# Optimization experiments

Hardware: AMD Instinct MI355X
Metric: run time of the kernel (lower is better)

## Reference

```python
import jax, jax.numpy as jnp
import numpy as np

B, IN, H = 4096, 1024, 1024


def setup_inputs() -> dict:
    key = jax.random.key(0)
    ks = jax.random.split(key, 12)
    s = float(np.sqrt(6.0 / (IN + H)))  # xavier-uniform-like scale
    u = lambda k, shp: jax.random.uniform(k, shp, jnp.float32, -s, s)
    return {
        "x": jax.random.normal(ks[0], (B, IN), jnp.float32),
        "h_prev": jax.random.normal(ks[1], (B, H), jnp.float32),
        "c_prev": jax.random.normal(ks[2], (B, H), jnp.float32),
        "n_prev": jnp.ones((B, H), jnp.float32),
        "m_prev": jnp.zeros((B, H), jnp.float32),
        "Wi_x": u(ks[3], (H, IN)), "bi": jnp.zeros((H,), jnp.float32), "Wi_h": u(ks[4], (H, H)),
        "Wf_x": u(ks[5], (H, IN)), "bf": jnp.full((H,), 2.0, jnp.float32), "Wf_h": u(ks[6], (H, H)),
        "Wz_x": u(ks[7], (H, IN)), "bz": jnp.zeros((H,), jnp.float32), "Wz_h": u(ks[8], (H, H)),
        "Wo_x": u(ks[9], (H, IN)), "bo": jnp.zeros((H,), jnp.float32), "Wo_h": u(ks[10], (H, H)),
    }


def reference(x, h_prev, c_prev, n_prev, m_prev,
              Wi_x, bi, Wi_h, Wf_x, bf, Wf_h,
              Wz_x, bz, Wz_h, Wo_x, bo, Wo_h):
    # 8 projections (x-side with bias, h-side without), torch Linear: y = x @ W.T + b
    i_tilde = x @ Wi_x.T + bi + h_prev @ Wi_h.T
    f_aff   = x @ Wf_x.T + bf + h_prev @ Wf_h.T
    z_aff   = x @ Wz_x.T + bz + h_prev @ Wz_h.T
    o_aff   = x @ Wo_x.T + bo + h_prev @ Wo_h.T

    # forget_as_exp=False path: sigmoid forget gate, log-domain stabilizer
    log_f = jnp.log(jnp.clip(jax.nn.sigmoid(f_aff), 1e-8, None))
    m_t = jnp.maximum(log_f + m_prev, i_tilde)
    i_prime = jnp.exp(i_tilde - m_t)
    f_prime = jnp.exp(log_f + m_prev - m_t)

    z = jnp.tanh(z_aff)
    c_t = f_prime * c_prev + i_prime * z
    n_t = f_prime * n_prev + i_prime
    h_t = jax.nn.sigmoid(o_aff) * (c_t / jnp.clip(n_t, 1e-6, None))
    return h_t, c_t, n_t, m_t
```

## Files before the change

### kernel.cpp

```cpp
#include <hip/hip_runtime.h>
#include <stdint.h>


#define B_DIM 4096
#define K_DIM 2048

typedef __bf16 bf16x8 __attribute__((ext_vector_type(8)));
typedef float f32x4 __attribute__((ext_vector_type(4)));
typedef unsigned short ushort8 __attribute__((ext_vector_type(8)));

__device__ __forceinline__ unsigned short f2bf(float f) {
  unsigned u = __float_as_uint(f);
  u += 0x7fffu + ((u >> 16) & 1u);
  return (unsigned short)(u >> 16);
}
__device__ __forceinline__ float bf2f(unsigned short u) {
  return __uint_as_float(((unsigned)u) << 16);
}

__device__ __forceinline__ ushort8 load8_as_bf16(const void* base, size_t off, bool isbf) {
  if (isbf) return *(const ushort8*)((const unsigned short*)base + off);
  const float* f = (const float*)base + off;
  float4 v0 = ((const float4*)f)[0];
  float4 v1 = ((const float4*)f)[1];
  ushort8 o;
  o[0] = f2bf(v0.x); o[1] = f2bf(v0.y); o[2] = f2bf(v0.z); o[3] = f2bf(v0.w);
  o[4] = f2bf(v1.x); o[5] = f2bf(v1.y); o[6] = f2bf(v1.z); o[7] = f2bf(v1.w);
  return o;
}

__global__ void pack_all(const void* __restrict__ xv, const void* __restrict__ hv,
                         const void* __restrict__ Wix, const void* __restrict__ Wih,
                         const void* __restrict__ Wfx, const void* __restrict__ Wfh,
                         const void* __restrict__ Wzx, const void* __restrict__ Wzh,
                         const void* __restrict__ Wox, const void* __restrict__ Woh,
                         unsigned short* __restrict__ Apk, unsigned short* __restrict__ Bpk) {
  const int blk = blockIdx.x;
  const int lane = threadIdx.x & 63;
  const bool isA = blk < 4096;
  const unsigned* disc = (const unsigned*)(isA ? xv : Wix);
  int v = 0;
  if (lane < 32) {
    unsigned e = (disc[lane] >> 7) & 0xFFu;
    v = (e > (isA ? 129u : 122u)) ? 1 : 0;
  }
  const bool isbf = (__ballot(v) == 0ull);

  const int k = threadIdx.x * 8;
  if (isA) {
    const int m = blk;
    const void* src = (k < 1024) ? xv : hv;
    size_t off = (size_t)m * 1024 + (k & 1023);
    *(ushort8*)(Apk + (size_t)m * 2048 + k) = load8_as_bf16(src, off, isbf);
  } else {
    const int br = blk - 4096;
    const int g = (br >> 4) & 3;
    const int wrow = ((br >> 6) << 4) | (br & 15);
    const void* W;
    if (k < 1024) W = (g == 0) ? Wix : (g == 1) ? Wfx : (g == 2) ? Wzx : Wox;
    else          W = (g == 0) ? Wih : (g == 1) ? Wfh : (g == 2) ? Wzh : Woh;
    size_t off = (size_t)wrow * 1024 + (k & 1023);
    *(ushort8*)(Bpk + (size_t)br * 2048 + k) = load8_as_bf16(W, off, isbf);
  }
}


__device__ __forceinline__ void gload16(const unsigned short* g, unsigned short* l) {
  __builtin_amdgcn_global_load_lds(
      (__attribute__((address_space(1))) void*)g,
      (__attribute__((address_space(3))) void*)l, 16, 0, 0);
}

#define SCHED0 __builtin_amdgcn_sched_barrier(0)
#define BAR    __builtin_amdgcn_s_barrier()
#define VM6    asm volatile("s_waitcnt vmcnt(6)" ::: "memory")
#define VM0    asm volatile("s_waitcnt vmcnt(0)" ::: "memory")
#define LGKM(N) asm volatile("s_waitcnt lgkmcnt(" #N ")" ::: "memory")
#define NOWAIT ((void)0)
#define NOSTAGE ((void)0)

#define STAGE_HALF(buf, ab, hf, kt) {                                          \
    _Pragma("unroll")                                                          \
    for (int r_ = 0; r_ < 2; ++r_) {                                           \
      const unsigned short* g_ = (ab ? sB : sA) +                              \
          (size_t)((r_ * 128 + (hf) * (ab ? 32 : 64)) * 2048 + (kt) * 64);     \
      gload16(g_, &lds[buf][ab][(hf) * 128 + r_ * 64 + w * 8][0]);             \
    } }

#define LDSA(buf, mh, mi, CS) \
  (*(const bf16x8*)(&lds[buf][0][0][0] + ((mh)*128 + (mi)*16)*64 + aBase + CS))
#define LDSB(buf, nh, nf, CS) \
  (*(const bf16x8*)(&lds[buf][1][0][0] + ((nh)*128 + (nf)*16)*64 + bBase + CS))

#define RD16(buf) {                                                            \
    fA[0][0]=LDSA(buf,0,0,csw0); fA[1][0]=LDSA(buf,0,1,csw0);                  \
    fA[2][0]=LDSA(buf,0,2,csw0); fA[3][0]=LDSA(buf,0,3,csw0);                  \
    fB0[0][0]=LDSB(buf,0,0,csw0); fB0[1][0]=LDSB(buf,0,1,csw0);                \
    SCHED0;                                                                    \
    fA[0][1]=LDSA(buf,0,0,csw1); fA[1][1]=LDSA(buf,0,1,csw1);                  \
    fA[2][1]=LDSA(buf,0,2,csw1); fA[3][1]=LDSA(buf,0,3,csw1);                  \
    fB0[0][1]=LDSB(buf,0,0,csw1); fB0[1][1]=LDSB(buf,0,1,csw1);                \
    SCHED0;                                                                    \
    fB1[0][0]=LDSB(buf,1,0,csw0); fB1[1][0]=LDSB(buf,1,1,csw0);                \
    fB1[0][1]=LDSB(buf,1,0,csw1); fB1[1][1]=LDSB(buf,1,1,csw1);                \
  }

#define MFMA_H(FB, MH, NH, KS) {                                               \
    __builtin_amdgcn_s_setprio(1);                                             \
    _Pragma("unroll") for (int mi = 0; mi < 4; ++mi)                           \
      _Pragma("unroll") for (int nf = 0; nf < 2; ++nf)                         \
        acc[(MH)*4+mi][(NH)*2+nf] = __builtin_amdgcn_mfma_f32_16x16x32_bf16(   \
            fA[mi][KS], FB[nf][KS], acc[(MH)*4+mi][(NH)*2+nf], 0, 0, 0);       \
    __builtin_amdgcn_s_setprio(0); }

#define MFMA_Q2(FB, MH, NH) {                                                  \
    __builtin_amdgcn_s_setprio(1);                                             \
    _Pragma("unroll") for (int mi = 0; mi < 4; ++mi)                           \
      _Pragma("unroll") for (int nf = 0; nf < 2; ++nf)                         \
        _Pragma("unroll") for (int ks = 0; ks < 2; ++ks)                       \
          acc[(MH)*4+mi][(NH)*2+nf] = __builtin_amdgcn_mfma_f32_16x16x32_bf16( \
              fA[mi][ks], FB[nf][ks], acc[(MH)*4+mi][(NH)*2+nf], 0, 0, 0);     \
    __builtin_amdgcn_s_setprio(0); }

#define PHASE1(buf, STG) {                                                     \
    RD16(buf); SCHED0; STG; SCHED0; BAR;                                       \
    LGKM(10); SCHED0;                                                          \
    MFMA_H(fB0, 0, 0, 0); SCHED0;                                              \
    LGKM(4); SCHED0;                                                           \
    MFMA_H(fB0, 0, 0, 1); SCHED0;                                              \
    BAR; SCHED0; }

#define PHASE2(buf, STG) {                                                     \
    STG; SCHED0; BAR;                                                          \
    LGKM(0); SCHED0;                                                           \
    __builtin_amdgcn_s_setprio(1);                                             \
    _Pragma("unroll") for (int mi = 0; mi < 4; ++mi) {                         \
      _Pragma("unroll") for (int nf = 0; nf < 2; ++nf)                         \
        _Pragma("unroll") for (int ks = 0; ks < 2; ++ks)                       \
          acc[mi][2+nf] = __builtin_amdgcn_mfma_f32_16x16x32_bf16(             \
              fA[mi][ks], fB1[nf][ks], acc[mi][2+nf], 0, 0, 0);                \
      fA[mi][0] = LDSA(buf, 1, mi, csw0);                                      \
      fA[mi][1] = LDSA(buf, 1, mi, csw1);                                      \
    }                                                                          \
    __builtin_amdgcn_s_setprio(0); SCHED0;                                     \
    BAR; SCHED0; }

#define PHASE3(STG) {                                                          \
    STG; SCHED0; BAR;                                                          \
    LGKM(0); SCHED0;                                                           \
    MFMA_Q2(fB1, 1, 1); SCHED0;                                                \
    BAR; SCHED0; }

#define PHASE4(STG, VMW) {                                                     \
    STG; SCHED0; BAR;                                                          \
    LGKM(0); SCHED0;                                                           \
    MFMA_Q2(fB0, 1, 0); VMW; SCHED0;                                           \
    BAR; SCHED0; }

__global__ __launch_bounds__(512, 2) void gemm_fused(
    const unsigned short* __restrict__ Apk,
    const unsigned short* __restrict__ Bpk,
    const void* __restrict__ bi, const void* __restrict__ bfg,
    const void* __restrict__ bz, const void* __restrict__ bo,
    const void* __restrict__ c_prev, const void* __restrict__ n_prev,
    const void* __restrict__ m_prev,
    float* __restrict__ out)
{
  __shared__ unsigned short lds[2][2][256][64];

  const int tid  = threadIdx.x;
  const int w    = tid >> 6;
  const int lane = tid & 63;
  const int wm   = w >> 2;
  const int wn   = w & 3;
  const int lcol = lane & 15;

  const int bid = blockIdx.x;
  const int swz = (bid & 7) * 32 + (bid >> 3);
  const int bm = swz >> 4;
  const int bn = swz & 15;

  const int l3 = lane >> 3;
  const int cg = (lane & 7) ^ l3;
  const unsigned short* sA = Apk + (size_t)(bm * 256 + w * 8 + l3) * 2048 + cg * 8;
  const unsigned short* sB = Bpk + (size_t)(bn * 256 + (w >> 2) * 64 + (w & 3) * 8 + l3) * 2048 + cg * 8;

  const int csw0 = (((lane >> 4)    ) ^ (lane & 7)) * 8;
  const int csw1 = ((4 + (lane >> 4)) ^ (lane & 7)) * 8;
  const int aBase = (wm * 64 + lcol) * 64;
  const int bBase = (wn * 32 + lcol) * 64;

  f32x4 acc[8][4] = {};
  bf16x8 fA[4][2], fB0[2][2], fB1[2][2];

  STAGE_HALF(0, 0, 0, 0); SCHED0;
  STAGE_HALF(0, 1, 0, 0); SCHED0;
  STAGE_HALF(0, 1, 1, 0); SCHED0;
  STAGE_HALF(0, 0, 1, 0); SCHED0;
  STAGE_HALF(1, 0, 0, 1); SCHED0;
  STAGE_HALF(1, 1, 0, 1); SCHED0;
  STAGE_HALF(1, 1, 1, 1); SCHED0;
  VM6; SCHED0; BAR; SCHED0;

  for (int t = 0; t < 30; t += 2) {
    PHASE1(0, STAGE_HALF(1, 0, 1, t + 1));
    PHASE2(0, STAGE_HALF(0, 0, 0, t + 2));
    PHASE3(   STAGE_HALF(0, 1, 0, t + 2));
    PHASE4(   STAGE_HALF(0, 1, 1, t + 2), VM6);
    PHASE1(1, STAGE_HALF(0, 0, 1, t + 2));
    PHASE2(1, STAGE_HALF(1, 0, 0, t + 3));
    PHASE3(   STAGE_HALF(1, 1, 0, t + 3));
    PHASE4(   STAGE_HALF(1, 1, 1, t + 3), VM6);
  }
  PHASE1(0, STAGE_HALF(1, 0, 1, 31));
  PHASE2(0, NOSTAGE);
  PHASE3(   NOSTAGE);
  PHASE4(   NOSTAGE, VM0);
  PHASE1(1, NOSTAGE);
  PHASE2(1, NOSTAGE);
  PHASE3(   NOSTAGE);
  PHASE4(   NOSTAGE, NOWAIT);

  const bool sbf = (((const unsigned*)n_prev)[0] == 0x3F803F80u);
  const bool bbf = (((const unsigned*)bfg)[0]    == 0x40004000u);
  const int n = (bn * 4 + wn) * 16 + lcol;
  const float bi_n = bbf ? bf2f(((const unsigned short*)bi)[n])  : ((const float*)bi)[n];
  const float bf_n = bbf ? bf2f(((const unsigned short*)bfg)[n]) : ((const float*)bfg)[n];
  const float bz_n = bbf ? bf2f(((const unsigned short*)bz)[n])  : ((const float*)bz)[n];
  const float bo_n = bbf ? bf2f(((const unsigned short*)bo)[n])  : ((const float*)bo)[n];
  const int row0 = bm * 256 + wm * 128 + (lane >> 4) * 4;

  float* out_h = out;
  float* out_c = out + 4194304;
  float* out_n = out + 2 * 4194304;
  float* out_m = out + 3 * 4194304;

#pragma unroll
  for (int mi = 0; mi < 8; ++mi) {
#pragma unroll
    for (int r = 0; r < 4; ++r) {
      const int row = row0 + mi * 16 + r;
      const size_t idx = (size_t)row * 1024 + n;
      float it = acc[mi][0][r] + bi_n;
      float fa = acc[mi][1][r] + bf_n;
      float za = acc[mi][2][r] + bz_n;
      float oa = acc[mi][3][r] + bo_n;
      float cp  = sbf ? bf2f(((const unsigned short*)c_prev)[idx]) : ((const float*)c_prev)[idx];
      float npv = sbf ? bf2f(((const unsigned short*)n_prev)[idx]) : ((const float*)n_prev)[idx];
      float mp  = sbf ? bf2f(((const unsigned short*)m_prev)[idx]) : ((const float*)m_prev)[idx];

      float sf = 1.f / (1.f + __expf(-fa));
      sf = fmaxf(sf, 1e-8f);
      float lf = __logf(sf);
      float mt = fmaxf(lf + mp, it);
      float ip = __expf(it - mt);
      float fp = __expf(lf + mp - mt);
      float zc = fminf(fmaxf(za, -15.f), 15.f);
      float e2 = __expf(2.f * zc);
      float z  = (e2 - 1.f) / (e2 + 1.f);
      float ct = fp * cp + ip * z;
      float nt = fp * npv + ip;
      float so = 1.f / (1.f + __expf(-oa));
      float ht = so * (ct / fmaxf(nt, 1e-6f));

      out_h[idx] = ht;
      out_c[idx] = ct;
      out_n[idx] = nt;
      out_m[idx] = mt;
    }
  }
}

extern "C" void kernel_launch(void* const* d_in, const int* in_sizes, int n_in,
                              void* d_out, int out_size, void* d_ws, size_t ws_size,
                              hipStream_t stream) {
  const void* x      = d_in[0];
  const void* h_prev = d_in[1];
  const void* c_prev = d_in[2];
  const void* n_prev = d_in[3];
  const void* m_prev = d_in[4];
  const void* Wi_x = d_in[5];
  const void* bi   = d_in[6];
  const void* Wi_h = d_in[7];
  const void* Wf_x = d_in[8];
  const void* bf   = d_in[9];
  const void* Wf_h = d_in[10];
  const void* Wz_x = d_in[11];
  const void* bz   = d_in[12];
  const void* Wz_h = d_in[13];
  const void* Wo_x = d_in[14];
  const void* bo   = d_in[15];
  const void* Wo_h = d_in[16];

  unsigned short* Apk = (unsigned short*)d_ws;
  unsigned short* Bpk = Apk + (size_t)B_DIM * K_DIM;

  pack_all<<<8192, 256, 0, stream>>>(x, h_prev, Wi_x, Wi_h, Wf_x, Wf_h,
                                     Wz_x, Wz_h, Wo_x, Wo_h, Apk, Bpk);
  gemm_fused<<<256, 512, 0, stream>>>(Apk, Bpk, bi, bf, bz, bo,
                                      c_prev, n_prev, m_prev,
                                      (float*)d_out);
}
```

Baseline: 256.2 us.

## Stage epilogue state loads and output stores through LDS for coalesced access

For fp32 state inputs, the epilogue now loads c_prev/n_prev/m_prev tiles into LDS with global_load_lds, builds the four output tiles in LDS, and writes them back with full 16-byte vector stores. Before, each lane did scattered 4-byte loads and stores with only 16 contiguous columns per row. Each half-tile pass adds several barriers and LDS round trips, and the output tile reuses the GEMM LDS buffer.

```diff
diff --git a/kernel.cpp b/kernel.cpp
--- a/kernel.cpp
+++ b/kernel.cpp
@@ -65,7 +65,7 @@
 }
 
 
-__device__ __forceinline__ void gload16(const unsigned short* g, unsigned short* l) {
+__device__ __forceinline__ void gload16(const void* g, void* l) {
   __builtin_amdgcn_global_load_lds(
       (__attribute__((address_space(1))) void*)g,
       (__attribute__((address_space(3))) void*)l, 16, 0, 0);
@@ -174,6 +174,7 @@
   const int wm   = w >> 2;
   const int wn   = w & 3;
   const int lcol = lane & 15;
+  const int qrow = lane >> 4;
 
   const int bid = blockIdx.x;
   const int swz = (bid & 7) * 32 + (bid >> 3);
@@ -223,52 +224,123 @@
 
   const bool sbf = (((const unsigned*)n_prev)[0] == 0x3F803F80u);
   const bool bbf = (((const unsigned*)bfg)[0]    == 0x40004000u);
-  const int n = (bn * 4 + wn) * 16 + lcol;
+  const int bcol = wn * 16 + lcol;
+  const int n = bn * 64 + bcol;
   const float bi_n = bbf ? bf2f(((const unsigned short*)bi)[n])  : ((const float*)bi)[n];
   const float bf_n = bbf ? bf2f(((const unsigned short*)bfg)[n]) : ((const float*)bfg)[n];
   const float bz_n = bbf ? bf2f(((const unsigned short*)bz)[n])  : ((const float*)bz)[n];
   const float bo_n = bbf ? bf2f(((const unsigned short*)bo)[n])  : ((const float*)bo)[n];
-  const int row0 = bm * 256 + wm * 128 + (lane >> 4) * 4;
-
-  float* out_h = out;
-  float* out_c = out + 4194304;
-  float* out_n = out + 2 * 4194304;
-  float* out_m = out + 3 * 4194304;
-
-#pragma unroll
-  for (int mi = 0; mi < 8; ++mi) {
-#pragma unroll
-    for (int r = 0; r < 4; ++r) {
-      const int row = row0 + mi * 16 + r;
-      const size_t idx = (size_t)row * 1024 + n;
-      float it = acc[mi][0][r] + bi_n;
-      float fa = acc[mi][1][r] + bf_n;
-      float za = acc[mi][2][r] + bz_n;
-      float oa = acc[mi][3][r] + bo_n;
-      float cp  = sbf ? bf2f(((const unsigned short*)c_prev)[idx]) : ((const float*)c_prev)[idx];
-      float npv = sbf ? bf2f(((const unsigned short*)n_prev)[idx]) : ((const float*)n_prev)[idx];
-      float mp  = sbf ? bf2f(((const unsigned short*)m_prev)[idx]) : ((const float*)m_prev)[idx];
-
-      float sf = 1.f / (1.f + __expf(-fa));
-      sf = fmaxf(sf, 1e-8f);
-      float lf = __logf(sf);
-      float mt = fmaxf(lf + mp, it);
-      float ip = __expf(it - mt);
-      float fp = __expf(lf + mp - mt);
-      float zc = fminf(fmaxf(za, -15.f), 15.f);
-      float e2 = __expf(2.f * zc);
-      float z  = (e2 - 1.f) / (e2 + 1.f);
-      float ct = fp * cp + ip * z;
-      float nt = fp * npv + ip;
-      float so = 1.f / (1.f + __expf(-oa));
+
+#define GATE_MATH                                                              \
+      float sf = 1.f / (1.f + __expf(-fa));                                    \
+      sf = fmaxf(sf, 1e-8f);                                                   \
+      float lf_ = __logf(sf);                                                  \
+      float mt = fmaxf(lf_ + mp, it);                                          \
+      float ip = __expf(it - mt);                                              \
+      float fp = __expf(lf_ + mp - mt);                                        \
+      float zc = fminf(fmaxf(za, -15.f), 15.f);                                \
+      float e2 = __expf(2.f * zc);                                             \
+      float z  = (e2 - 1.f) / (e2 + 1.f);                                      \
+      float ct = fp * cp + ip * z;                                             \
+      float nt = fp * npv + ip;                                                \
+      float so = 1.f / (1.f + __expf(-oa));                                    \
       float ht = so * (ct / fmaxf(nt, 1e-6f));
 
-      out_h[idx] = ht;
-      out_c[idx] = ct;
-      out_n[idx] = nt;
-      out_m[idx] = mt;
+  if (!sbf) {
+    float* lf = (float*)&lds[0][0][0][0];
+    const float* srcC = (const float*)c_prev;
+    const float* srcN = (const float*)n_prev;
+    const float* srcM = (const float*)m_prev;
+
+#pragma unroll
+    for (int hh = 0; hh < 2; ++hh) {
+#pragma unroll
+      for (int s = 0; s < 3; ++s) {
+        const float* srcp = (s == 0) ? srcC : (s == 1) ? srcN : srcM;
+#pragma unroll
+        for (int jj = 0; jj < 4; ++jj) {
+          const int j = w * 4 + jj;
+          const int lr = j * 4 + qrow;
+          const int grow = bm * 256 + (lr >> 6) * 128 + hh * 64 + (lr & 63);
+          const float* g = srcp + (size_t)grow * 1024 + bn * 64 + lcol * 4;
+          gload16(g, lf + s * 8192 + j * 256);
+        }
+      }
+      SCHED0; VM0; SCHED0; BAR; SCHED0;
+
+      float gc[16], gn[16], gm[16];
+#pragma unroll
+      for (int ml = 0; ml < 4; ++ml)
+#pragma unroll
+        for (int r = 0; r < 4; ++r) {
+          const int off = (wm * 64 + ml * 16 + qrow * 4 + r) * 64 + bcol;
+          gc[ml * 4 + r] = lf[off];
+          gn[ml * 4 + r] = lf[8192 + off];
+          gm[ml * 4 + r] = lf[16384 + off];
+        }
+      SCHED0; LGKM(0); SCHED0; BAR; SCHED0;
+
+#pragma unroll
+      for (int ml = 0; ml < 4; ++ml) {
+        const int mi = hh * 4 + ml;
+#pragma unroll
+        for (int r = 0; r < 4; ++r) {
+          const int e = ml * 4 + r;
+          float it = acc[mi][0][r] + bi_n;
+          float fa = acc[mi][1][r] + bf_n;
+          float za = acc[mi][2][r] + bz_n;
+          float oa = acc[mi][3][r] + bo_n;
+          float cp = gc[e], npv = gn[e], mp = gm[e];
+          GATE_MATH
+          const int off = (wm * 64 + ml * 16 + qrow * 4 + r) * 64 + bcol;
+          lf[off]         = ht;
+          lf[8192  + off] = ct;
+          lf[16384 + off] = nt;
+          lf[24576 + off] = mt;
+        }
+      }
+      SCHED0; LGKM(0); SCHED0; BAR; SCHED0;
+
+#pragma unroll
+      for (int k = 0; k < 16; ++k) {
+        const int c = k * 512 + tid;
+        const int s = c >> 11;
+        const int cs = c & 2047;
+        const int lr = cs >> 4, c4 = cs & 15;
+        f32x4 v = *(const f32x4*)(lf + s * 8192 + lr * 64 + c4 * 4);
+        const int grow = bm * 256 + (lr >> 6) * 128 + hh * 64 + (lr & 63);
+        *(f32x4*)(out + (size_t)s * 4194304 + (size_t)grow * 1024 + bn * 64 + c4 * 4) = v;
+      }
+      SCHED0; LGKM(0); SCHED0; BAR; SCHED0;
     }
-  }
+  } else {
+    const int row0 = bm * 256 + wm * 128 + qrow * 4;
+    float* out_h = out;
+    float* out_c = out + 4194304;
+    float* out_n = out + 2 * 4194304;
+    float* out_m = out + 3 * 4194304;
+#pragma unroll
+    for (int mi = 0; mi < 8; ++mi) {
+#pragma unroll
+      for (int r = 0; r < 4; ++r) {
+        const int row = row0 + mi * 16 + r;
+        const size_t idx = (size_t)row * 1024 + n;
+        float it = acc[mi][0][r] + bi_n;
+        float fa = acc[mi][1][r] + bf_n;
+        float za = acc[mi][2][r] + bz_n;
+        float oa = acc[mi][3][r] + bo_n;
+        float cp  = bf2f(((const unsigned short*)c_prev)[idx]);
+        float npv = bf2f(((const unsigned short*)n_prev)[idx]);
+        float mp  = bf2f(((const unsigned short*)m_prev)[idx]);
+        GATE_MATH
+        out_h[idx] = ht;
+        out_c[idx] = ct;
+        out_n[idx] = nt;
+        out_m[idx] = mt;
+      }
+    }
+  }
+#undef GATE_MATH
 }
 
 extern "C" void kernel_launch(void* const* d_in, const int* in_sizes, int n_in,
```

Result: faster. 249.9 us (-2.5%).
